# Kernel tuning notes

Hardware: AMD Instinct MI355X
Metric: run time of the kernel (lower is better)

## Reference

```python
import jax, jax.numpy as jnp
import numpy as np

HEADS = 20
HEAD_DIM = 64
NUM_TOKENS = 4


def _split_heads(x, B):
    # (B, S, H*D) -> (B, H, S, D)
    return x.reshape(B, -1, HEADS, HEAD_DIM).transpose(0, 2, 1, 3)


def setup_inputs() -> dict:
    key = jax.random.key(0)
    ks = jax.random.split(key, 10)
    B, HW, hid, cad, Ltxt = 2, 4096, 1280, 2048, 77
    w = lambda k, shp: (jax.random.normal(k, shp, jnp.float32) * 0.02)
    return {
        "hidden_states": jax.random.normal(ks[0], (B, HW, hid), jnp.float32),
        "encoder_hidden_states": jax.random.normal(ks[1], (B, Ltxt + NUM_TOKENS, cad), jnp.float32),
        "indices_to_alter": jax.random.randint(ks[2], (B,), 0, Ltxt, jnp.int32),
        "Wq": w(ks[3], (hid, hid)),
        "Wk": w(ks[4], (cad, hid)),
        "Wv": w(ks[5], (cad, hid)),
        "Wk_nest": w(ks[6], (cad, hid)),
        "Wv_nest": w(ks[7], (cad, hid)),
        "Wout": w(ks[8], (hid, hid)),
        "b_out": jnp.zeros((hid,), jnp.float32),
    }


def reference(hidden_states, encoder_hidden_states, indices_to_alter,
              Wq, Wk, Wv, Wk_nest, Wv_nest, Wout, b_out):
    B, HW, _ = hidden_states.shape
    end = encoder_hidden_states.shape[1] - NUM_TOKENS
    txt = encoder_hidden_states[:, :end]   # (B, Ltxt, cad)
    img = encoder_hidden_states[:, end:]   # (B, num_tokens, cad)

    q = _split_heads(hidden_states @ Wq, B)   # (B, H, HW, D)
    k = _split_heads(txt @ Wk, B)             # (B, H, Lt, D)
    v = _split_heads(txt @ Wv, B)             # (B, H, Lt, D)
    kn = _split_heads(img @ Wk_nest, B)       # (B, H, T, D)
    vn = _split_heads(img @ Wv_nest, B)       # (B, H, T, D)

    sc = 1.0 / jnp.sqrt(jnp.float32(HEAD_DIM))

    # nested attention: per-spatial-position identity value V* (SDPA over image tokens)
    wn = jax.nn.softmax(jnp.einsum('bhqd,bhkd->bhqk', q, kn) * sc, axis=-1)
    value_id = jnp.einsum('bhqk,bhkd->bhqd', wn, vn)          # (B, H, HW, D)

    # main cross attention over text tokens
    w = jax.nn.softmax(jnp.einsum('bhqd,bhkd->bhqk', q, k) * sc, axis=-1)  # (B,H,HW,Lt)
    base = jnp.einsum('bhqk,bhkd->bhqd', w, v)                # (B, H, HW, D)

    # V_mixed[b,h,i] differs from value only at text slot s_b, where it equals value_id[b,h,i].
    # sum_k w[...,k] * V_mixed[...,k,:] == w @ v + w[...,s]*(value_id - v[:, :, s])
    s = indices_to_alter
    w_s = jnp.take_along_axis(w, s[:, None, None, None], axis=3)   # (B, H, HW, 1)
    v_s = jnp.take_along_axis(v, s[:, None, None, None], axis=2)   # (B, H, 1, D)
    out = base + w_s * (value_id - v_s)                             # (B, H, HW, D)

    out = out.transpose(0, 2, 1, 3).reshape(B, HW, HEADS * HEAD_DIM)
    return out @ Wout + b_out
```

## Files before the change

### kernel.cpp

```cpp
#include <hip/hip_runtime.h>
#include <hip/hip_bf16.h>


typedef unsigned short ushort_t;
typedef __attribute__((ext_vector_type(8))) short short8;
typedef __attribute__((ext_vector_type(4))) float f32x4;

#define B_   2
#define HW_  4096
#define HID_ 1280
#define CAD_ 2048
#define LTXT 77
#define NTOK 4
#define NH_  20
#define HD_  64

__device__ __forceinline__ ushort_t f2bf(float f) {
    __hip_bfloat16 h = __float2bfloat16(f);
    return *reinterpret_cast<ushort_t*>(&h);
}

__device__ __forceinline__ void gld_lds16(const void* g, void* l) {
    __builtin_amdgcn_global_load_lds(
        (const __attribute__((address_space(1))) unsigned int*)g,
        (__attribute__((address_space(3))) unsigned int*)l,
        16, 0, 0);
}

__global__ __launch_bounds__(256) void prep(
    const float* __restrict__ hs, const float* __restrict__ enc,
    const float* __restrict__ s0, const float* __restrict__ s1,
    const float* __restrict__ s2, const float* __restrict__ s3,
    const float* __restrict__ s4, const float* __restrict__ s5,
    ushort_t* __restrict__ hsb, ushort_t* __restrict__ encb,
    ushort_t* __restrict__ d0, ushort_t* __restrict__ d1,
    ushort_t* __restrict__ d2, ushort_t* __restrict__ d3,
    ushort_t* __restrict__ d4, ushort_t* __restrict__ d5)
{
    const int y = blockIdx.y, t = threadIdx.x;
    if (y <= 1) {
        const float* src = y ? enc : hs;
        ushort_t* dst = y ? encb : hsb;
        int n4 = y ? (B_ * (LTXT + NTOK) * CAD_) / 4 : (B_ * HW_ * HID_) / 4;
        int step = gridDim.x * 256;
        for (int i = blockIdx.x * 256 + t; i < n4; i += step) {
            float4 v = *(const float4*)(src + (size_t)i * 4);
            ushort_t o[4] = { f2bf(v.x), f2bf(v.y), f2bf(v.z), f2bf(v.w) };
            *(uint2*)(dst + (size_t)i * 4) = *(uint2*)o;
        }
        return;
    }
    int z = y - 2;
    const float* S; ushort_t* D; int K_;
    switch (z) {
        case 0: S = s0; D = d0; K_ = 1280; break;
        case 1: S = s1; D = d1; K_ = 2048; break;
        case 2: S = s2; D = d2; K_ = 2048; break;
        case 3: S = s3; D = d3; K_ = 2048; break;
        case 4: S = s4; D = d4; K_ = 2048; break;
        default: S = s5; D = d5; K_ = 1280; break;
    }
    int tr = blockIdx.x / 40, tc = blockIdx.x % 40;
    if (tr >= K_ / 32) return;
    __shared__ ushort_t tl[32][33];
    int c = t & 31, r0 = t >> 5;
#pragma unroll
    for (int i = 0; i < 4; i++) {
        int r = r0 + i * 8;
        tl[r][c] = f2bf(S[(size_t)(tr * 32 + r) * 1280 + tc * 32 + c]);
    }
    __syncthreads();
#pragma unroll
    for (int i = 0; i < 4; i++) {
        int r = r0 + i * 8;
        D[(size_t)(tc * 32 + r) * K_ + tr * 32 + c] = tl[c][r];
    }
}

template <bool F32OUT>
__device__ __forceinline__ void gemm_body(
    const ushort_t* __restrict__ A, const ushort_t* __restrict__ Bt,
    void* __restrict__ Cout, const float* __restrict__ biasf,
    int M, int K, int lda, int row0, int col0)
{
    __shared__ ushort_t lsA[128 * 32];
    __shared__ ushort_t lsB[128 * 32];
    const int t = threadIdx.x;
    const int w = t >> 6, l = t & 63;
    const int mb = (w >> 1) * 64, nb = (w & 1) * 64;
    const int lrow = l & 15, lk = (l >> 4) * 8;
    f32x4 acc[4][4] = {};
    for (int k0 = 0; k0 < K; k0 += 32) {
        __syncthreads();
#pragma unroll
        for (int p = 0; p < 2; p++) {
            int lin = p * 256 + t;
            int r = lin >> 2, cc = (lin & 3) * 8;
            int ra = row0 + r; if (ra > M - 1) ra = M - 1;
            gld_lds16(A + (size_t)ra * lda + k0 + cc, &lsA[lin * 8]);
            int rb = col0 + r;
            gld_lds16(Bt + (size_t)rb * K + k0 + cc, &lsB[lin * 8]);
        }
        __syncthreads();
        short8 af[4], bfr[4];
#pragma unroll
        for (int mt = 0; mt < 4; mt++)
            af[mt] = *(const short8*)&lsA[(mb + mt * 16 + lrow) * 32 + lk];
#pragma unroll
        for (int nt = 0; nt < 4; nt++)
            bfr[nt] = *(const short8*)&lsB[(nb + nt * 16 + lrow) * 32 + lk];
#pragma unroll
        for (int mt = 0; mt < 4; mt++)
#pragma unroll
            for (int nt = 0; nt < 4; nt++)
                acc[mt][nt] = __builtin_amdgcn_mfma_f32_16x16x32_bf16(
                    af[mt], bfr[nt], acc[mt][nt], 0, 0, 0);
    }
    const int quad = l >> 4, cl = l & 15;
#pragma unroll
    for (int nt = 0; nt < 4; nt++) {
        int col = col0 + nb + nt * 16 + cl;
        float bv = biasf ? biasf[col] : 0.f;
#pragma unroll
        for (int mt = 0; mt < 4; mt++)
#pragma unroll
            for (int r = 0; r < 4; r++) {
                int row = row0 + mb + mt * 16 + quad * 4 + r;
                if (row < M) {
                    if (F32OUT)
                        ((float*)Cout)[(size_t)row * 1280 + col] = acc[mt][nt][r] + bv;
                    else
                        ((ushort_t*)Cout)[(size_t)row * 1280 + col] = f2bf(acc[mt][nt][r] + bv);
                }
            }
    }
}

__global__ __launch_bounds__(256, 3) void gemm_q_kv(
    const ushort_t* __restrict__ hsb, const ushort_t* __restrict__ encb,
    const ushort_t* __restrict__ WqT,
    const ushort_t* __restrict__ WkT, const ushort_t* __restrict__ WvT,
    const ushort_t* __restrict__ WknT, const ushort_t* __restrict__ WvnT,
    ushort_t* __restrict__ qb, ushort_t* __restrict__ kb, ushort_t* __restrict__ vb,
    ushort_t* __restrict__ knb, ushort_t* __restrict__ vnb)
{
    int x = blockIdx.x, col0 = blockIdx.y * 128;
    if (x < 64) {
        gemm_body<false>(hsb, WqT, qb, nullptr, B_ * HW_, HID_, HID_, x * 128, col0);
        return;
    }
    int z = x - 64, kind = z & 1;
    const ushort_t* A; const ushort_t* Bt; ushort_t* C; int M;
    if (z < 4) {
        int bb = z >> 1;
        M = LTXT;
        A = encb + (size_t)bb * (LTXT + NTOK) * CAD_;
        Bt = kind ? WvT : WkT;
        C = (kind ? vb : kb) + (size_t)bb * LTXT * HID_;
    } else {
        int bb = (z - 4) >> 1;
        M = NTOK;
        A = encb + ((size_t)bb * (LTXT + NTOK) + LTXT) * CAD_;
        Bt = kind ? WvnT : WknT;
        C = (kind ? vnb : knb) + (size_t)bb * NTOK * HID_;
    }
    gemm_body<false>(A, Bt, C, nullptr, M, CAD_, CAD_, 0, col0);
}

__global__ __launch_bounds__(256, 3) void gemm_bt_f32(
    const ushort_t* __restrict__ A, const ushort_t* __restrict__ Bt,
    float* __restrict__ C, const float* __restrict__ biasf, int M, int K, int lda)
{
    gemm_body<true>(A, Bt, C, biasf, M, K, lda, blockIdx.x * 128, blockIdx.y * 128);
}

__global__ __launch_bounds__(256, 3) void attn_kernel(
    const ushort_t* __restrict__ qb, const ushort_t* __restrict__ kbf,
    const ushort_t* __restrict__ vbf, const ushort_t* __restrict__ knb,
    const ushort_t* __restrict__ vnb, const int* __restrict__ sidx,
    ushort_t* __restrict__ ob)
{
    const int qt = blockIdx.x, h = blockIdx.y, b = blockIdx.z;
    const int t = threadIdx.x, w = t >> 6, l = t & 63;
    const int s_idx = sidx[b];
    __shared__ ushort_t Kl[96 * 72];
    __shared__ ushort_t VT[64 * 104];
    __shared__ ushort_t QP[128 * 104];

    for (int id = t; id < 96 * 8; id += 256) {
        int key = id >> 3, c = (id & 7) * 8;
        uint4 v;
        if (key < LTXT)
            v = *(const uint4*)&kbf[((size_t)(b * LTXT + key)) * HID_ + h * HD_ + c];
        else if (key >= 80 && key < 80 + NTOK)
            v = *(const uint4*)&knb[((size_t)(b * NTOK + key - 80)) * HID_ + h * HD_ + c];
        else
            v = make_uint4(0u, 0u, 0u, 0u);
        *(uint4*)&Kl[key * 72 + c] = v;
    }
    for (int id = t; id < 64 * 96; id += 256) {
        int d = id / 96, key = id - d * 96;
        ushort_t val = 0;
        if (key < LTXT)
            val = vbf[((size_t)(b * LTXT + key)) * HID_ + h * HD_ + d];
        else if (key >= 80 && key < 80 + NTOK)
            val = vnb[((size_t)(b * NTOK + key - 80)) * HID_ + h * HD_ + d];
        VT[d * 104 + key] = val;
    }
    const int q0 = qt * 128;
    for (int id = t; id < 128 * 8; id += 256) {
        int r = id >> 3, c = (id & 7) * 8;
        uint4 v = *(const uint4*)&qb[((size_t)(b * HW_ + q0 + r)) * HID_ + h * HD_ + c];
        *(uint4*)&QP[r * 72 + c] = v;
    }
    __syncthreads();

    const int mbw = w * 32, lrow = l & 15, lk = (l >> 4) * 8;
    const int quad = l >> 4, cl = l & 15;

    f32x4 S[2][6] = {};
#pragma unroll
    for (int ks = 0; ks < 2; ks++) {
        short8 af0 = *(const short8*)&QP[(mbw + lrow) * 72 + ks * 32 + lk];
        short8 af1 = *(const short8*)&QP[(mbw + 16 + lrow) * 72 + ks * 32 + lk];
#pragma unroll
        for (int nt = 0; nt < 6; nt++) {
            short8 bf = *(const short8*)&Kl[(nt * 16 + lrow) * 72 + ks * 32 + lk];
            S[0][nt] = __builtin_amdgcn_mfma_f32_16x16x32_bf16(af0, bf, S[0][nt], 0, 0, 0);
            S[1][nt] = __builtin_amdgcn_mfma_f32_16x16x32_bf16(af1, bf, S[1][nt], 0, 0, 0);
        }
    }
    __syncthreads();

    const float sc = 0.125f;
#pragma unroll
    for (int mt = 0; mt < 2; mt++) {
#pragma unroll
        for (int r = 0; r < 4; r++) {
            float v[6];
#pragma unroll
            for (int nt = 0; nt < 6; nt++) v[nt] = S[mt][nt][r] * sc;
            float m = -1e30f;
#pragma unroll
            for (int nt = 0; nt < 5; nt++) {
                int c = nt * 16 + cl;
                if (c < LTXT) m = fmaxf(m, v[nt]);
            }
#pragma unroll
            for (int off = 1; off < 16; off <<= 1) m = fmaxf(m, __shfl_xor(m, off));
            float e[5], lsum = 0.f, wsn = 0.f;
#pragma unroll
            for (int nt = 0; nt < 5; nt++) {
                int c = nt * 16 + cl;
                float ev = (c < LTXT) ? __expf(v[nt] - m) : 0.f;
                e[nt] = ev; lsum += ev;
                if (c == s_idx) wsn += ev;
            }
#pragma unroll
            for (int off = 1; off < 16; off <<= 1) {
                lsum += __shfl_xor(lsum, off);
                wsn  += __shfl_xor(wsn, off);
            }
            float inv = 1.f / lsum;
            float ws = wsn * inv;
            bool nv = (cl < 4);
            float m5 = nv ? v[5] : -1e30f;
#pragma unroll
            for (int off = 1; off < 16; off <<= 1) m5 = fmaxf(m5, __shfl_xor(m5, off));
            float e5 = nv ? __expf(v[5] - m5) : 0.f;
            float l5 = e5;
#pragma unroll
            for (int off = 1; off < 16; off <<= 1) l5 += __shfl_xor(l5, off);
            float p5 = ws * e5 / l5;
            int row = mbw + mt * 16 + quad * 4 + r;
#pragma unroll
            for (int nt = 0; nt < 5; nt++) {
                int c = nt * 16 + cl;
                float p = (c < LTXT && c != s_idx) ? e[nt] * inv : 0.f;
                QP[row * 104 + c] = f2bf(p);
            }
            QP[row * 104 + 80 + cl] = f2bf(p5);
        }
    }
    __syncthreads();

    f32x4 O[2][4] = {};
#pragma unroll
    for (int ks = 0; ks < 3; ks++) {
        short8 af0 = *(const short8*)&QP[(mbw + lrow) * 104 + ks * 32 + lk];
        short8 af1 = *(const short8*)&QP[(mbw + 16 + lrow) * 104 + ks * 32 + lk];
#pragma unroll
        for (int nt = 0; nt < 4; nt++) {
            short8 bf = *(const short8*)&VT[(nt * 16 + lrow) * 104 + ks * 32 + lk];
            O[0][nt] = __builtin_amdgcn_mfma_f32_16x16x32_bf16(af0, bf, O[0][nt], 0, 0, 0);
            O[1][nt] = __builtin_amdgcn_mfma_f32_16x16x32_bf16(af1, bf, O[1][nt], 0, 0, 0);
        }
    }
#pragma unroll
    for (int mt = 0; mt < 2; mt++)
#pragma unroll
        for (int nt = 0; nt < 4; nt++)
#pragma unroll
            for (int r = 0; r < 4; r++) {
                int row = mbw + mt * 16 + quad * 4 + r;
                int d = nt * 16 + cl;
                ob[((size_t)(b * HW_ + q0 + row)) * HID_ + h * HD_ + d] = f2bf(O[mt][nt][r]);
            }
}

extern "C" void kernel_launch(void* const* d_in, const int* in_sizes, int n_in,
                              void* d_out, int out_size, void* d_ws, size_t ws_size,
                              hipStream_t stream) {
    const float* hs   = (const float*)d_in[0];
    const float* enc  = (const float*)d_in[1];
    const int*   idx  = (const int*)d_in[2];
    const float* Wq   = (const float*)d_in[3];
    const float* Wk   = (const float*)d_in[4];
    const float* Wv   = (const float*)d_in[5];
    const float* Wkn  = (const float*)d_in[6];
    const float* Wvn  = (const float*)d_in[7];
    const float* Wout = (const float*)d_in[8];
    const float* bout = (const float*)d_in[9];
    float* out = (float*)d_out;

    ushort_t* ws = (ushort_t*)d_ws;
    size_t o = 0;
    ushort_t* WqT   = ws + o; o += (size_t)1280 * 1280;
    ushort_t* WkT   = ws + o; o += (size_t)1280 * 2048;
    ushort_t* WvT   = ws + o; o += (size_t)1280 * 2048;
    ushort_t* WknT  = ws + o; o += (size_t)1280 * 2048;
    ushort_t* WvnT  = ws + o; o += (size_t)1280 * 2048;
    ushort_t* WoutT = ws + o; o += (size_t)1280 * 1280;
    ushort_t* hsb   = ws + o; o += (size_t)B_ * HW_ * HID_;
    ushort_t* encb  = ws + o; o += (size_t)B_ * (LTXT + NTOK) * CAD_;
    ushort_t* qbuf  = ws + o; o += (size_t)B_ * HW_ * HID_;
    ushort_t* kbuf  = ws + o; o += (size_t)B_ * LTXT * HID_;
    ushort_t* vbuf  = ws + o; o += (size_t)B_ * LTXT * HID_;
    ushort_t* knbuf = ws + o; o += (size_t)B_ * NTOK * HID_;
    ushort_t* vnbuf = ws + o; o += (size_t)B_ * NTOK * HID_;
    ushort_t* attnb = hsb;

    prep<<<dim3(2560, 8), 256, 0, stream>>>(hs, enc, Wq, Wk, Wv, Wkn, Wvn, Wout,
                                            hsb, encb,
                                            WqT, WkT, WvT, WknT, WvnT, WoutT);
    gemm_q_kv<<<dim3(72, 10), 256, 0, stream>>>(hsb, encb, WqT, WkT, WvT, WknT, WvnT,
                                                qbuf, kbuf, vbuf, knbuf, vnbuf);
    attn_kernel<<<dim3(HW_ / 128, NH_, B_), 256, 0, stream>>>(qbuf, kbuf, vbuf,
                                                              knbuf, vnbuf, idx, attnb);
    gemm_bt_f32<<<dim3(64, 10), 256, 0, stream>>>(attnb, WoutT, out, bout,
                                                  B_ * HW_, HID_, HID_);
}
```

Before: 286.2 us.

## Double-buffer LDS tiles in GEMM to overlap global loads with MFMA

After: 290.5 us. No clear change (+1.5%).

```diff
diff --git a/kernel.cpp b/kernel.cpp
--- a/kernel.cpp
+++ b/kernel.cpp
@@ -83,39 +83,59 @@
     void* __restrict__ Cout, const float* __restrict__ biasf,
     int M, int K, int lda, int row0, int col0)
 {
-    __shared__ ushort_t lsA[128 * 32];
-    __shared__ ushort_t lsB[128 * 32];
+    __shared__ ushort_t lsA[2][128 * 32];
+    __shared__ ushort_t lsB[2][128 * 32];
     const int t = threadIdx.x;
     const int w = t >> 6, l = t & 63;
     const int mb = (w >> 1) * 64, nb = (w & 1) * 64;
     const int lrow = l & 15, lk = (l >> 4) * 8;
+
+    const int r0s = t >> 2, c0s = (t & 3) * 8;
+    const int r1s = r0s + 64;
+    const ushort_t* Arow0; const ushort_t* Arow1;
+    {
+        int ra0 = row0 + r0s; if (ra0 > M - 1) ra0 = M - 1;
+        int ra1 = row0 + r1s; if (ra1 > M - 1) ra1 = M - 1;
+        Arow0 = A + (size_t)ra0 * lda + c0s;
+        Arow1 = A + (size_t)ra1 * lda + c0s;
+    }
+    const ushort_t* Brow0 = Bt + (size_t)(col0 + r0s) * K + c0s;
+    const ushort_t* Brow1 = Bt + (size_t)(col0 + r1s) * K + c0s;
+
     f32x4 acc[4][4] = {};
+
+    gld_lds16(Arow0, &lsA[0][(t) * 8]);
+    gld_lds16(Arow1, &lsA[0][(256 + t) * 8]);
+    gld_lds16(Brow0, &lsB[0][(t) * 8]);
+    gld_lds16(Brow1, &lsB[0][(256 + t) * 8]);
+    __syncthreads();
+
+    int cur = 0;
     for (int k0 = 0; k0 < K; k0 += 32) {
-        __syncthreads();
-#pragma unroll
-        for (int p = 0; p < 2; p++) {
-            int lin = p * 256 + t;
-            int r = lin >> 2, cc = (lin & 3) * 8;
-            int ra = row0 + r; if (ra > M - 1) ra = M - 1;
-            gld_lds16(A + (size_t)ra * lda + k0 + cc, &lsA[lin * 8]);
-            int rb = col0 + r;
-            gld_lds16(Bt + (size_t)rb * K + k0 + cc, &lsB[lin * 8]);
-        }
-        __syncthreads();
+        int nxt = cur ^ 1;
+        if (k0 + 32 < K) {
+            gld_lds16(Arow0 + k0 + 32, &lsA[nxt][(t) * 8]);
+            gld_lds16(Arow1 + k0 + 32, &lsA[nxt][(256 + t) * 8]);
+            gld_lds16(Brow0 + k0 + 32, &lsB[nxt][(t) * 8]);
+            gld_lds16(Brow1 + k0 + 32, &lsB[nxt][(256 + t) * 8]);
+        }
         short8 af[4], bfr[4];
 #pragma unroll
         for (int mt = 0; mt < 4; mt++)
-            af[mt] = *(const short8*)&lsA[(mb + mt * 16 + lrow) * 32 + lk];
+            af[mt] = *(const short8*)&lsA[cur][(mb + mt * 16 + lrow) * 32 + lk];
 #pragma unroll
         for (int nt = 0; nt < 4; nt++)
-            bfr[nt] = *(const short8*)&lsB[(nb + nt * 16 + lrow) * 32 + lk];
+            bfr[nt] = *(const short8*)&lsB[cur][(nb + nt * 16 + lrow) * 32 + lk];
 #pragma unroll
         for (int mt = 0; mt < 4; mt++)
 #pragma unroll
             for (int nt = 0; nt < 4; nt++)
                 acc[mt][nt] = __builtin_amdgcn_mfma_f32_16x16x32_bf16(
                     af[mt], bfr[nt], acc[mt][nt], 0, 0, 0);
-    }
+        __syncthreads();
+        cur = nxt;
+    }
+
     const int quad = l >> 4, cl = l & 15;
 #pragma unroll
     for (int nt = 0; nt < 4; nt++) {
```

## Double-buffer LDS tiles in GEMM and enlarge per-wave tile to 64x128

Applied to the files above, without the earlier changes.

Result: slower. 300.0 us (+4.8%).

```diff
diff --git a/kernel.cpp b/kernel.cpp
--- a/kernel.cpp
+++ b/kernel.cpp
@@ -83,49 +83,69 @@
     void* __restrict__ Cout, const float* __restrict__ biasf,
     int M, int K, int lda, int row0, int col0)
 {
-    __shared__ ushort_t lsA[128 * 32];
-    __shared__ ushort_t lsB[128 * 32];
+    __shared__ ushort_t lsA[2][128 * 32];
+    __shared__ ushort_t lsB[2][128 * 32];
     const int t = threadIdx.x;
     const int w = t >> 6, l = t & 63;
-    const int mb = (w >> 1) * 64, nb = (w & 1) * 64;
     const int lrow = l & 15, lk = (l >> 4) * 8;
-    f32x4 acc[4][4] = {};
+
+    const int rs = t >> 2, cs = (t & 3) * 8;
+    const ushort_t* Asrc[4];
+    const ushort_t* Bsrc[4];
+#pragma unroll
+    for (int j = 0; j < 4; j++) {
+        int ra = row0 + rs + 32 * j; if (ra > M - 1) ra = M - 1;
+        Asrc[j] = A + (size_t)ra * lda + cs;
+        Bsrc[j] = Bt + (size_t)(col0 + rs + 32 * j) * K + cs;
+    }
+    const int ldst = rs * 32 + cs;
+
+    f32x4 acc[4][8] = {};
+
+#pragma unroll
+    for (int j = 0; j < 4; j++) {
+        gld_lds16(Asrc[j], &lsA[0][ldst + j * 1024]);
+        gld_lds16(Bsrc[j], &lsB[0][ldst + j * 1024]);
+    }
+    __syncthreads();
+
+    int cur = 0;
     for (int k0 = 0; k0 < K; k0 += 32) {
-        __syncthreads();
-#pragma unroll
-        for (int p = 0; p < 2; p++) {
-            int lin = p * 256 + t;
-            int r = lin >> 2, cc = (lin & 3) * 8;
-            int ra = row0 + r; if (ra > M - 1) ra = M - 1;
-            gld_lds16(A + (size_t)ra * lda + k0 + cc, &lsA[lin * 8]);
-            int rb = col0 + r;
-            gld_lds16(Bt + (size_t)rb * K + k0 + cc, &lsB[lin * 8]);
-        }
-        __syncthreads();
-        short8 af[4], bfr[4];
+        int nxt = cur ^ 1;
+        if (k0 + 32 < K) {
+#pragma unroll
+            for (int j = 0; j < 4; j++) {
+                gld_lds16(Asrc[j] + k0 + 32, &lsA[nxt][ldst + j * 1024]);
+                gld_lds16(Bsrc[j] + k0 + 32, &lsB[nxt][ldst + j * 1024]);
+            }
+        }
+        short8 af[4], bfr[8];
 #pragma unroll
         for (int mt = 0; mt < 4; mt++)
-            af[mt] = *(const short8*)&lsA[(mb + mt * 16 + lrow) * 32 + lk];
-#pragma unroll
-        for (int nt = 0; nt < 4; nt++)
-            bfr[nt] = *(const short8*)&lsB[(nb + nt * 16 + lrow) * 32 + lk];
+            af[mt] = *(const short8*)&lsA[cur][(w * 64 + mt * 16 + lrow) * 32 + lk];
+#pragma unroll
+        for (int nt = 0; nt < 8; nt++)
+            bfr[nt] = *(const short8*)&lsB[cur][(nt * 16 + lrow) * 32 + lk];
 #pragma unroll
         for (int mt = 0; mt < 4; mt++)
 #pragma unroll
-            for (int nt = 0; nt < 4; nt++)
+            for (int nt = 0; nt < 8; nt++)
                 acc[mt][nt] = __builtin_amdgcn_mfma_f32_16x16x32_bf16(
                     af[mt], bfr[nt], acc[mt][nt], 0, 0, 0);
-    }
+        __syncthreads();
+        cur = nxt;
+    }
+
     const int quad = l >> 4, cl = l & 15;
 #pragma unroll
-    for (int nt = 0; nt < 4; nt++) {
-        int col = col0 + nb + nt * 16 + cl;
+    for (int nt = 0; nt < 8; nt++) {
+        int col = col0 + nt * 16 + cl;
         float bv = biasf ? biasf[col] : 0.f;
 #pragma unroll
         for (int mt = 0; mt < 4; mt++)
 #pragma unroll
             for (int r = 0; r < 4; r++) {
-                int row = row0 + mb + mt * 16 + quad * 4 + r;
+                int row = row0 + w * 64 + mt * 16 + quad * 4 + r;
                 if (row < M) {
                     if (F32OUT)
                         ((float*)Cout)[(size_t)row * 1280 + col] = acc[mt][nt][r] + bv;
@@ -136,7 +156,7 @@
     }
 }
 
-__global__ __launch_bounds__(256, 3) void gemm_q_kv(
+__global__ __launch_bounds__(128, 2) void gemm_q_kv(
     const ushort_t* __restrict__ hsb, const ushort_t* __restrict__ encb,
     const ushort_t* __restrict__ WqT,
     const ushort_t* __restrict__ WkT, const ushort_t* __restrict__ WvT,
@@ -167,7 +187,7 @@
     gemm_body<false>(A, Bt, C, nullptr, M, CAD_, CAD_, 0, col0);
 }
 
-__global__ __launch_bounds__(256, 3) void gemm_bt_f32(
+__global__ __launch_bounds__(128, 2) void gemm_bt_f32(
     const ushort_t* __restrict__ A, const ushort_t* __restrict__ Bt,
     float* __restrict__ C, const float* __restrict__ biasf, int M, int K, int lda)
 {
@@ -343,10 +363,10 @@
     prep<<<dim3(2560, 8), 256, 0, stream>>>(hs, enc, Wq, Wk, Wv, Wkn, Wvn, Wout,
                                             hsb, encb,
                                             WqT, WkT, WvT, WknT, WvnT, WoutT);
-    gemm_q_kv<<<dim3(72, 10), 256, 0, stream>>>(hsb, encb, WqT, WkT, WvT, WknT, WvnT,
+    gemm_q_kv<<<dim3(72, 10), 128, 0, stream>>>(hsb, encb, WqT, WkT, WvT, WknT, WvnT,
                                                 qbuf, kbuf, vbuf, knbuf, vnbuf);
     attn_kernel<<<dim3(HW_ / 128, NH_, B_), 256, 0, stream>>>(qbuf, kbuf, vbuf,
                                                               knbuf, vnbuf, idx, attnb);
-    gemm_bt_f32<<<dim3(64, 10), 256, 0, stream>>>(attnb, WoutT, out, bout,
+    gemm_bt_f32<<<dim3(64, 10), 128, 0, stream>>>(attnb, WoutT, out, bout,
                                                   B_ * HW_, HID_, HID_);
 }
```
